# Optimization experiments

Hardware: AMD Instinct MI355X
Metric: run time of the kernel (lower is better)

## Reference

```python
import jax, jax.numpy as jnp
import numpy as np

NUM_ITERATIONS = 3
LN_EPS = 1e-5


def setup_inputs() -> dict:
    key = jax.random.key(0)
    ks = jax.random.split(key, 10)
    B, L, Lv, H = 8, 2048, 256, 1024
    s = 1.0 / np.sqrt(H)
    s2 = 1.0 / np.sqrt(2 * H)
    return {
        "text_feat": jax.random.normal(ks[0], (B, L, H), dtype=jnp.float32),
        "vision_feat": jax.random.normal(ks[1], (B, Lv, H), dtype=jnp.float32),
        "Wt": jax.random.uniform(ks[2], (H, H), jnp.float32, -s, s),
        "bt": jax.random.uniform(ks[3], (H,), jnp.float32, -s, s),
        "Wv": jax.random.uniform(ks[4], (H, H), jnp.float32, -s, s),
        "bv": jax.random.uniform(ks[5], (H,), jnp.float32, -s, s),
        "Wg": jax.random.uniform(ks[6], (H, 2 * H), jnp.float32, -s2, s2),
        "bg": jax.random.uniform(ks[7], (H,), jnp.float32, -s2, s2),
        "gamma": jnp.ones((H,), jnp.float32),
        "beta": jnp.zeros((H,), jnp.float32),
    }


def reference(text_feat, vision_feat, Wt, bt, Wv, bv, Wg, bg, gamma, beta):
    B, L, H = text_feat.shape
    # mean-pool vision over its sequence, broadcast over L
    vision_pooled = jnp.mean(vision_feat, axis=1, keepdims=True)          # [B,1,H]
    text_proj = jnp.einsum('blh,oh->blo', text_feat, Wt) + bt             # [B,L,H]
    vision_proj = jnp.einsum('bkh,oh->bko', vision_pooled, Wv) + bv       # [B,1,H]
    vision_proj = jnp.broadcast_to(vision_proj, (B, L, H))                # expand to [B,L,H]

    # agreement is loop-invariant in the original code; compute once
    agreement = jnp.sum(text_proj * vision_proj, axis=-1, keepdims=True)  # [B,L,1]

    coupling = jnp.zeros((B, L, 1), dtype=text_feat.dtype)
    fused = text_feat
    for _ in range(NUM_ITERATIONS):
        routing_weights = jax.nn.softmax(coupling, axis=1)                # softmax over L
        weighted_vision = routing_weights * vision_proj                   # [B,L,H]
        # gate = sigmoid(Linear(concat(text_proj, weighted_vision)))
        Wg_t, Wg_v = Wg[:, :H], Wg[:, H:]
        gate_pre = (jnp.einsum('blh,oh->blo', text_proj, Wg_t)
                    + jnp.einsum('blh,oh->blo', weighted_vision, Wg_v) + bg)
        gate = jax.nn.sigmoid(gate_pre)
        fused = text_feat + gate * weighted_vision
        coupling = coupling + agreement

    # LayerNorm over last dim (dropout is identity in eval)
    mu = jnp.mean(fused, axis=-1, keepdims=True)
    var = jnp.mean(jnp.square(fused - mu), axis=-1, keepdims=True)
    out = (fused - mu) / jnp.sqrt(var + LN_EPS) * gamma + beta
    return out
```

## Files before the change

kernel.cpp:

```cpp
#include <hip/hip_runtime.h>
#include <hip/hip_bf16.h>
#include <hip/hip_fp8.h>

typedef __bf16 bf16_t;
typedef bf16_t bf16x4 __attribute__((ext_vector_type(4)));
typedef bf16_t bf16x8 __attribute__((ext_vector_type(8)));
typedef float  f32x4  __attribute__((ext_vector_type(4)));

#define B_  8
#define L_  2048
#define H_  1024
#define LV_ 256

typedef const __attribute__((address_space(1))) void* gptr_as1;
typedef __attribute__((address_space(3))) void* lptr_as3;

__device__ __forceinline__ void gload_lds16(void* lds_base, const void* gsrc) {
  __builtin_amdgcn_global_load_lds((gptr_as1)gsrc, (lptr_as3)lds_base, 16, 0, 0);
}
__device__ __forceinline__ void gload_lds4(void* lds_base, const void* gsrc) {
  __builtin_amdgcn_global_load_lds((gptr_as1)gsrc, (lptr_as3)lds_base, 4, 0, 0);
}

__device__ __forceinline__ unsigned char to_fp8(float x) {
  return __hip_fp8_e4m3(x).__x;
}

__global__ __launch_bounds__(256) void vpool64(const float* __restrict__ vf,
                                               float* __restrict__ pooled) {
  __shared__ float part[256];
  int bid = blockIdx.x;
  int b = bid >> 3, hc = bid & 7;
  int t = threadIdx.x;
  int h = hc * 128 + (t & 127);
  int kh = t >> 7;
  const float* p = vf + (long)b * (LV_ * H_) + (long)kh * 128 * H_ + h;
  float s = 0.f;
  #pragma unroll 4
  for (int k = 0; k < 128; ++k) s += p[k * H_];
  part[t] = s;
  __syncthreads();
  if (t < 128)
    pooled[b * H_ + hc * 128 + t] = (part[t] + part[t + 128]) * (1.f / 256.f);
}

__global__ void matvec8(const float* __restrict__ W, int ldw, int woff,
                        const float* __restrict__ x,
                        const float* __restrict__ bias,
                        float* __restrict__ out) {
  int wid = threadIdx.x >> 6, lane = threadIdx.x & 63;
  int o = blockIdx.x * 4 + wid;
  const float* wr = W + (long)o * ldw + woff;
  float acc[B_];
  #pragma unroll
  for (int b = 0; b < B_; ++b) acc[b] = 0.f;
  for (int j = 0; j < 16; ++j) {
    float w = wr[lane + 64 * j];
    #pragma unroll
    for (int b = 0; b < B_; ++b) acc[b] += w * x[b * H_ + lane + 64 * j];
  }
  #pragma unroll
  for (int b = 0; b < B_; ++b)
    for (int off = 32; off; off >>= 1) acc[b] += __shfl_down(acc[b], off);
  if (lane == 0) {
    float bb = bias ? bias[o] : 0.f;
    #pragma unroll
    for (int b = 0; b < B_; ++b) out[b * H_ + o] = acc[b] + bb;
  }
}

__global__ __launch_bounds__(256) void smallops(const float* __restrict__ Wg,
                                                const float* __restrict__ Wt,
                                                const float* __restrict__ vp,
                                                const float* __restrict__ bt,
                                                const float* __restrict__ bg,
                                                float* __restrict__ gv,
                                                float* __restrict__ partU,
                                                float* __restrict__ cbb) {
  int bid = blockIdx.x;
  if (bid < 256) {
    int wid = threadIdx.x >> 6, lane = threadIdx.x & 63;
    int o = bid * 4 + wid;
    const float* wr = Wg + (long)o * 2048 + 1024;
    float acc[B_];
    #pragma unroll
    for (int b = 0; b < B_; ++b) acc[b] = 0.f;
    for (int j = 0; j < 16; ++j) {
      float w = wr[lane + 64 * j];
      #pragma unroll
      for (int b = 0; b < B_; ++b) acc[b] += w * vp[b * H_ + lane + 64 * j];
    }
    #pragma unroll
    for (int b = 0; b < B_; ++b)
      for (int off = 32; off; off >>= 1) acc[b] += __shfl_down(acc[b], off);
    if (lane == 0) {
      #pragma unroll
      for (int b = 0; b < B_; ++b) gv[b * H_ + o] = acc[b];
    }
  } else if (bid < 512) {
    int lb = bid - 256;
    int e = (lb & 3) * 256 + threadIdx.x;
    int oc = lb >> 2;
    float a[B_];
    #pragma unroll
    for (int b = 0; b < B_; ++b) a[b] = 0.f;
    #pragma unroll
    for (int i = 0; i < 16; ++i) {
      int o = oc * 16 + i;
      float w = Wt[(long)o * H_ + e];
      #pragma unroll
      for (int b = 0; b < B_; ++b) a[b] += w * vp[b * H_ + o];
    }
    #pragma unroll
    for (int b = 0; b < B_; ++b) partU[oc * 8192 + b * 1024 + e] = a[b];
  } else {
    int lb = bid - 512;
    int wid = threadIdx.x >> 6, lane = threadIdx.x & 63;
    int o = lb * 4 + wid;
    const float* wr = Wg + (long)o * 2048;
    float acc = 0.f;
    for (int j = 0; j < 16; ++j) acc += wr[lane + 64 * j] * bt[lane + 64 * j];
    for (int off = 32; off; off >>= 1) acc += __shfl_down(acc, off);
    if (lane == 0) cbb[o] = acc + bg[o];
  }
}

__global__ __launch_bounds__(256) void reduceK(const float* __restrict__ src,
                                               float* __restrict__ dst,
                                               int nc, float scale) {
  int j = blockIdx.x * 256 + threadIdx.x;
  float s = 0.f;
  for (int c = 0; c < nc; ++c) s += src[c * 8192 + j];
  dst[j] = s * scale;
}

__global__ __launch_bounds__(256) void cvt_pack(const float* __restrict__ text,
                                                const float* __restrict__ u,
                                                const float* __restrict__ Wt,
                                                unsigned char* __restrict__ t8p,
                                                float* __restrict__ agr,
                                                bf16_t* __restrict__ WtT) {
  int bid = blockIdx.x;
  int t = threadIdx.x;
  if (bid < 1024) {
    __shared__ unsigned char q8[16][1032];
    __shared__ float dred[4][16];
    int b = bid >> 7;
    int wid = t >> 6, lane = t & 63;
    const float4* trow = (const float4*)(text + (long)bid * (16 * H_));
    float4 uu = ((const float4*)(u + b * H_))[t];
    #pragma unroll 4
    for (int i = 0; i < 16; ++i) {
      float4 v = trow[i * 256 + t];
      float d = v.x * uu.x + v.y * uu.y + v.z * uu.z + v.w * uu.w;
      for (int off = 32; off; off >>= 1) d += __shfl_down(d, off);
      if (!lane) dred[wid][i] = d;
      uchar4 q = { to_fp8(v.x), to_fp8(v.y), to_fp8(v.z), to_fp8(v.w) };
      *(uchar4*)&q8[i][t * 4] = q;
    }
    __syncthreads();
    if (t < 16)
      agr[bid * 16 + t] = dred[0][t] + dred[1][t] + dred[2][t] + dred[3][t];
    unsigned char* dst = t8p + (long)bid * 16384;
    #pragma unroll
    for (int c = 0; c < 8; ++c) {
      int kb = wid * 8 + c;
      uint2 r = *(const uint2*)&q8[lane & 15][kb * 32 + (lane >> 4) * 8];
      *(uint2*)(dst + kb * 512 + lane * 8) = r;
    }
  } else {
    __shared__ float tile[64][65];
    int lb = bid - 1024;
    int hr = (lb >> 4) * 64;
    int ec = (lb & 15) * 64;
    int lr = t >> 4, lc = t & 15;
    #pragma unroll
    for (int rr = 0; rr < 4; ++rr) {
      int r = rr * 16 + lr;
      float4 v = *(const float4*)(Wt + (long)(hr + r) * H_ + ec + lc * 4);
      tile[r][lc * 4 + 0] = v.x; tile[r][lc * 4 + 1] = v.y;
      tile[r][lc * 4 + 2] = v.z; tile[r][lc * 4 + 3] = v.w;
    }
    __syncthreads();
    #pragma unroll
    for (int rr = 0; rr < 4; ++rr) {
      int er = rr * 16 + lr;
      bf16x4 o = { (bf16_t)tile[lc * 4 + 0][er], (bf16_t)tile[lc * 4 + 1][er],
                   (bf16_t)tile[lc * 4 + 2][er], (bf16_t)tile[lc * 4 + 3][er] };
      *(bf16x4*)(WtT + (long)(ec + er) * H_ + hr + lc * 4) = o;
    }
  }
}

__global__ __launch_bounds__(256) void wc_sm(const float* __restrict__ Wg,
                                             const bf16_t* __restrict__ Bt,
                                             unsigned char* __restrict__ Cw8,
                                             const float* __restrict__ ag,
                                             float* __restrict__ r) {
  __shared__ __align__(16) char lds[2][16384];
  __shared__ float red[4];
  if (blockIdx.x >= 256) {
    int b = blockIdx.x - 256, t = threadIdx.x;
    int wid = t >> 6, lane = t & 63;
    const float* a = ag + (long)b * L_;
    float v[8];
    float mx = -1e30f;
    #pragma unroll
    for (int j = 0; j < 8; ++j) { v[j] = 2.f * a[t + 256 * j]; mx = fmaxf(mx, v[j]); }
    for (int off = 32; off; off >>= 1) mx = fmaxf(mx, __shfl_down(mx, off));
    if (!lane) red[wid] = mx;
    __syncthreads();
    mx = fmaxf(fmaxf(red[0], red[1]), fmaxf(red[2], red[3]));
    __syncthreads();
    float sum = 0.f;
    #pragma unroll
    for (int j = 0; j < 8; ++j) { v[j] = __expf(v[j] - mx); sum += v[j]; }
    for (int off = 32; off; off >>= 1) sum += __shfl_down(sum, off);
    if (!lane) red[wid] = sum;
    __syncthreads();
    sum = red[0] + red[1] + red[2] + red[3];
    float inv = 1.f / sum;
    #pragma unroll
    for (int j = 0; j < 8; ++j) r[(long)b * L_ + t + 256 * j] = v[j] * inv;
    return;
  }
  const int tid = threadIdx.x;
  const int wid = tid >> 6, lane = tid & 63;
  const int fr = lane & 15, fkb = (lane >> 4) * 16, fq = (lane >> 4) * 4;
  const int wm = wid >> 1, wn = wid & 1;
  const int tm = blockIdx.x & 15, tn = blockIdx.x >> 4;
  const int m0 = tm * 64, n0 = tn * 64;

  const int d0 = tid * 16;
  const int p  = d0 ^ (((d0 >> 7) & 7) << 4);
  const int rS = p >> 7, cS = (p & 127) >> 1;

  const int swz = (fr & 7) << 4;
  const int e0 = fkb ^ swz;
  const int e1 = (64 + fkb) ^ swz;

  auto stage = [&](int t) {
    char* base = lds[t & 1];
    gload_lds16(base + 8192 + d0,        Bt + (long)(n0 + rS) * H_ + t * 64 + cS);
    gload_lds16(base + 8192 + 4096 + d0, Bt + (long)(n0 + 32 + rS) * H_ + t * 64 + cS);
    const float* a0 = Wg + (long)(m0 + rS) * 2048 + t * 64 + cS;
    const float* a1 = Wg + (long)(m0 + 32 + rS) * 2048 + t * 64 + cS;
    float4 x0 = *(const float4*)a0, x1 = *(const float4*)(a0 + 4);
    float4 y0 = *(const float4*)a1, y1 = *(const float4*)(a1 + 4);
    bf16x8 bx = { (bf16_t)x0.x, (bf16_t)x0.y, (bf16_t)x0.z, (bf16_t)x0.w,
                  (bf16_t)x1.x, (bf16_t)x1.y, (bf16_t)x1.z, (bf16_t)x1.w };
    bf16x8 by = { (bf16_t)y0.x, (bf16_t)y0.y, (bf16_t)y0.z, (bf16_t)y0.w,
                  (bf16_t)y1.x, (bf16_t)y1.y, (bf16_t)y1.z, (bf16_t)y1.w };
    *(bf16x8*)(base + d0) = bx;
    *(bf16x8*)(base + 4096 + d0) = by;
  };

  f32x4 acc[2][2];
  #pragma unroll
  for (int m = 0; m < 2; ++m)
    #pragma unroll
    for (int n = 0; n < 2; ++n) acc[m][n] = (f32x4){0.f, 0.f, 0.f, 0.f};

  stage(0);
  __syncthreads();
  for (int t = 0; t < 16; ++t) {
    if (t + 1 < 16) stage(t + 1);
    char* buf = lds[t & 1];
    char* AR = buf + (wm * 32 + fr) * 128;
    char* BR = buf + 8192 + (wn * 32 + fr) * 128;
    bf16x8 a[2][2], b[2][2];
    #pragma unroll
    for (int m = 0; m < 2; ++m) {
      a[m][0] = *(const bf16x8*)(AR + m * 2048 + e0);
      a[m][1] = *(const bf16x8*)(AR + m * 2048 + e1);
      b[m][0] = *(const bf16x8*)(BR + m * 2048 + e0);
      b[m][1] = *(const bf16x8*)(BR + m * 2048 + e1);
    }
    #pragma unroll
    for (int m = 0; m < 2; ++m)
      #pragma unroll
      for (int n = 0; n < 2; ++n) {
        acc[m][n] = __builtin_amdgcn_mfma_f32_16x16x32_bf16(a[m][0], b[n][0], acc[m][n], 0, 0, 0);
        acc[m][n] = __builtin_amdgcn_mfma_f32_16x16x32_bf16(a[m][1], b[n][1], acc[m][n], 0, 0, 0);
      }
    __syncthreads();
  }
  #pragma unroll
  for (int m = 0; m < 2; ++m)
    #pragma unroll
    for (int r_ = 0; r_ < 4; ++r_) {
      int row = m0 + wm * 32 + m * 16 + fq + r_;
      #pragma unroll
      for (int n = 0; n < 2; ++n) {
        int col = n0 + wn * 32 + n * 16 + fr;
        Cw8[((row >> 4) * 32 + (col >> 5)) * 512
            + ((row & 15) + (((col >> 3) & 3) << 4)) * 8 + (col & 7)]
          = to_fp8(acc[m][n][r_] * 16.f);
      }
    }
}

#define BOFF 16777216
__global__ __launch_bounds__(512, 2)
void gemm_ln(const unsigned char* __restrict__ AB,
             const float* __restrict__ textf,
             const float* __restrict__ cbb, const float* __restrict__ rbuf,
             const float* __restrict__ gvb, const float* __restrict__ vpb,
             const float* __restrict__ gamma, const float* __restrict__ beta,
             float* __restrict__ out) {
  extern __shared__ __align__(16) char dlds[];
  const int tid  = threadIdx.x;
  const int w    = tid >> 6;
  const int lane = tid & 63;
  const int fr   = lane & 15;
  const int fq   = (lane >> 4) * 4;
  const int bid  = blockIdx.x;
  const long m0  = (long)bid * 64;
  const int bat  = (int)(m0 >> 11);

  const int o0 = tid * 4;
  const unsigned char* aSrc = AB + (long)bid * 65536 + (o0 >> 9) * 16384 + (o0 & 511);
  const unsigned char* bSrc = AB + BOFF + (long)(tid >> 5) * 16384 + (tid & 31) * 16;
  const int bD = (tid >> 5) * 512 + (tid & 31) * 16;

  {
    char* P = dlds + 104448;
    if (tid < 256) {
      gload_lds16(P + tid * 16,          cbb + tid * 4);
      gload_lds16(P + 8192 + tid * 16,   vpb + bat * H_ + tid * 4);
      gload_lds16(P + 16384 + tid * 16,  beta + tid * 4);
    } else {
      int t2 = tid - 256;
      gload_lds16(P + 4096 + t2 * 16,    gvb + bat * H_ + t2 * 4);
      gload_lds16(P + 12288 + t2 * 16,   gamma + t2 * 4);
    }
  }

  f32x4 acc[4][8];
  #pragma unroll
  for (int m = 0; m < 4; ++m)
    #pragma unroll
    for (int n = 0; n < 8; ++n) acc[m][n] = (f32x4){0.f, 0.f, 0.f, 0.f};

#define STAGE(t)                                                        \
  {                                                                     \
    gload_lds4(dlds + ((t) % 3) * 2048 + o0, aSrc + (t) * 512);         \
    _Pragma("unroll")                                                   \
    for (int r_ = 0; r_ < 4; ++r_)                                      \
      gload_lds16(dlds + 6144 + ((t) % 3) * 32768 + r_ * 8192 + bD,     \
                  bSrc + (long)r_ * 262144 + (t) * 512);                \
  }
#define KITER(t, WN)                                                    \
  {                                                                     \
    __builtin_amdgcn_sched_barrier(0);                                  \
    asm volatile("s_waitcnt vmcnt(" #WN ")" ::: "memory");              \
    __builtin_amdgcn_s_barrier();                                       \
    __builtin_amdgcn_sched_barrier(0);                                  \
    if ((t) + 2 < 32) STAGE((t) + 2)                                    \
    const char* Ab_ = dlds + ((t) % 3) * 2048 + lane * 8;               \
    const char* Bb_ = dlds + 6144 + ((t) % 3) * 32768 + w * 4096        \
                           + lane * 8;                                  \
    long a_[4], b_[8];                                                  \
    _Pragma("unroll")                                                   \
    for (int m_ = 0; m_ < 4; ++m_)                                      \
      a_[m_] = *(const long*)(Ab_ + m_ * 512);                          \
    _Pragma("unroll")                                                   \
    for (int n_ = 0; n_ < 8; ++n_)                                      \
      b_[n_] = *(const long*)(Bb_ + n_ * 512);                          \
    _Pragma("unroll")                                                   \
    for (int m_ = 0; m_ < 4; ++m_)                                      \
      _Pragma("unroll")                                                 \
      for (int n_ = 0; n_ < 8; ++n_)                                    \
        acc[m_][n_] = __builtin_amdgcn_mfma_f32_16x16x32_fp8_fp8(       \
            a_[m_], b_[n_], acc[m_][n_], 0, 0, 0);                      \
  }

  STAGE(0)
  asm volatile("" ::: "memory");
  STAGE(1)

  KITER(0, 5)  KITER(1, 5)  KITER(2, 5)  KITER(3, 5)
  KITER(4, 5)  KITER(5, 5)  KITER(6, 5)  KITER(7, 5)
  KITER(8, 5)  KITER(9, 5)  KITER(10, 5) KITER(11, 5)
  KITER(12, 5) KITER(13, 5) KITER(14, 5) KITER(15, 5)
  KITER(16, 5) KITER(17, 5) KITER(18, 5) KITER(19, 5)
  KITER(20, 5) KITER(21, 5) KITER(22, 5) KITER(23, 5)
  KITER(24, 5) KITER(25, 5) KITER(26, 5) KITER(27, 5)
  KITER(28, 5) KITER(29, 5) KITER(30, 5) KITER(31, 0)
#undef KITER
#undef STAGE

  const int lr = tid >> 5;
  const int jj = tid & 31;
  char* P = dlds + 104448;

  #pragma unroll
  for (int m = 0; m < 4; ++m) {
    __syncthreads();
    #pragma unroll
    for (int n = 0; n < 8; ++n) {
      #pragma unroll
      for (int r = 0; r < 4; ++r) {
        int rl = fq + r;
        int c  = (w * 128 + n * 16 + fr) ^ (((rl >> 2) & 3) << 4);
        *(float*)(dlds + rl * 4096 + c * 4) = acc[m][n][r];
      }
    }
    __syncthreads();
    long row = m0 + m * 16 + lr;
    float rv = rbuf[row];
    const float* tf = textf + row * H_;
    const int rot = ((lr >> 2) & 3) << 4;
    float s = 0.f, q = 0.f;
    #pragma unroll 2
    for (int k = 0; k < 8; ++k) {
      int c0 = k * 128 + jj * 4;
      char* slot = dlds + lr * 4096 + ((c0 ^ rot) * 4);
      f32x4 a4 = *(const f32x4*)slot;
      float4 t4  = *(const float4*)(tf + c0);
      f32x4 cb4 = *(const f32x4*)(P + c0 * 4);
      f32x4 gv4 = *(const f32x4*)(P + 4096 + c0 * 4);
      f32x4 vp4 = *(const f32x4*)(P + 8192 + c0 * 4);
      f32x4 f4;
      float gp, g;
      gp = a4[0] * 0.0625f + cb4[0] + rv * gv4[0];
      g = 1.f / (1.f + __expf(-gp));
      f4[0] = t4.x + g * rv * vp4[0];
      gp = a4[1] * 0.0625f + cb4[1] + rv * gv4[1];
      g = 1.f / (1.f + __expf(-gp));
      f4[1] = t4.y + g * rv * vp4[1];
      gp = a4[2] * 0.0625f + cb4[2] + rv * gv4[2];
      g = 1.f / (1.f + __expf(-gp));
      f4[2] = t4.z + g * rv * vp4[2];
      gp = a4[3] * 0.0625f + cb4[3] + rv * gv4[3];
      g = 1.f / (1.f + __expf(-gp));
      f4[3] = t4.w + g * rv * vp4[3];
      *(f32x4*)slot = f4;
      s += f4[0] + f4[1] + f4[2] + f4[3];
      q += f4[0] * f4[0] + f4[1] * f4[1] + f4[2] * f4[2] + f4[3] * f4[3];
    }
    #pragma unroll
    for (int off = 1; off < 32; off <<= 1) {
      s += __shfl_xor(s, off);
      q += __shfl_xor(q, off);
    }
    float mu  = s * (1.f / H_);
    float var = q * (1.f / H_) - mu * mu;
    float inv = rsqrtf(var + 1e-5f);
    float* op = out + row * H_;
    #pragma unroll 2
    for (int k = 0; k < 8; ++k) {
      int c0 = k * 128 + jj * 4;
      f32x4 f4 = *(const f32x4*)(dlds + lr * 4096 + ((c0 ^ rot) * 4));
      f32x4 gg = *(const f32x4*)(P + 12288 + c0 * 4);
      f32x4 bb = *(const f32x4*)(P + 16384 + c0 * 4);
      float4 o4;
      o4.x = (f4[0] - mu) * inv * gg[0] + bb[0];
      o4.y = (f4[1] - mu) * inv * gg[1] + bb[1];
      o4.z = (f4[2] - mu) * inv * gg[2] + bb[2];
      o4.w = (f4[3] - mu) * inv * gg[3] + bb[3];
      *(float4*)(op + c0) = o4;
    }
  }
}

extern "C" void kernel_launch(void* const* d_in, const int* in_sizes, int n_in,
                              void* d_out, int out_size, void* d_ws, size_t ws_size,
                              hipStream_t stream) {
  const float* text  = (const float*)d_in[0];
  const float* vis   = (const float*)d_in[1];
  const float* Wt    = (const float*)d_in[2];
  const float* bt    = (const float*)d_in[3];
  const float* Wv    = (const float*)d_in[4];
  const float* bv    = (const float*)d_in[5];
  const float* Wg    = (const float*)d_in[6];
  const float* bg    = (const float*)d_in[7];
  const float* gamma = (const float*)d_in[8];
  const float* beta  = (const float*)d_in[9];
  float* out = (float*)d_out;

  char* ws = (char*)d_ws;
  unsigned char* t8p   = (unsigned char*)(ws);
  unsigned char* Wc8p  = (unsigned char*)(ws + (size_t)16777216);
  bf16_t* WtT_b = (bf16_t*)(ws + (size_t)17825792);
  float*  pooled = (float*)(ws + (size_t)19922944);
  float*  vp     = (float*)(ws + (size_t)19955712);
  float*  gv     = (float*)(ws + (size_t)19988480);
  float*  u      = (float*)(ws + (size_t)20021248);
  float*  cbb    = (float*)(ws + (size_t)20054016);
  float*  rbuf   = (float*)(ws + (size_t)20058112);
  float*  agr    = (float*)(ws + (size_t)20123648);
  float*  partU  = (float*)(ws + (size_t)20189184);

  static bool smem_set = false;
  if (!smem_set) {
    (void)hipFuncSetAttribute((const void*)gemm_ln,
                              hipFuncAttributeMaxDynamicSharedMemorySize, 125184);
    smem_set = true;
  }

  vpool64<<<64, 256, 0, stream>>>(vis, pooled);
  matvec8<<<256, 256, 0, stream>>>(Wv, 1024, 0, pooled, bv, vp);
  smallops<<<768, 256, 0, stream>>>(Wg, Wt, vp, bt, bg, gv, partU, cbb);
  reduceK<<<32, 256, 0, stream>>>(partU, u, 64, 1.f);

  cvt_pack<<<1280, 256, 0, stream>>>(text, u, Wt, t8p, agr, WtT_b);
  wc_sm<<<264, 256, 0, stream>>>(Wg, WtT_b, Wc8p, agr, rbuf);

  gemm_ln<<<256, 512, 125184, stream>>>(t8p, text, cbb, rbuf, gv, vp,
                                        gamma, beta, out);
}
```

Measured before the change: 120.4 us.

## Merge prep kernels, use atomics for u, fold softmax into GEMM epilogue

Cuts the launch chain from seven kernels to five. The Wt transpose and the cbb bias dot move into the same launch as vision pooling, and that launch also zeroes u. The partial sums for u are now accumulated with atomicAdd, which removes the reduceK kernel and the partU buffer. The fp8 packing of text and the Wc GEMM share one launch, and each gemm_ln block recomputes its batch's softmax over agreement from agr instead of reading a precomputed routing buffer. The aim is to remove launch and serialization overhead. The costs are redundant softmax work in every GEMM block, atomic contention on u, and an order-dependent float sum.

```diff
diff --git a/kernel.cpp b/kernel.cpp
--- a/kernel.cpp
+++ b/kernel.cpp
@@ -26,22 +26,65 @@
   return __hip_fp8_e4m3(x).__x;
 }
 
-__global__ __launch_bounds__(256) void vpool64(const float* __restrict__ vf,
-                                               float* __restrict__ pooled) {
-  __shared__ float part[256];
+__global__ __launch_bounds__(256) void prep1(const float* __restrict__ vf,
+                                             const float* __restrict__ Wt,
+                                             const float* __restrict__ Wg,
+                                             const float* __restrict__ bt,
+                                             const float* __restrict__ bg,
+                                             float* __restrict__ pooled,
+                                             bf16_t* __restrict__ WtT,
+                                             float* __restrict__ cbb,
+                                             float* __restrict__ u) {
+  __shared__ __align__(16) char shm[16640];
   int bid = blockIdx.x;
-  int b = bid >> 3, hc = bid & 7;
   int t = threadIdx.x;
-  int h = hc * 128 + (t & 127);
-  int kh = t >> 7;
-  const float* p = vf + (long)b * (LV_ * H_) + (long)kh * 128 * H_ + h;
-  float s = 0.f;
-  #pragma unroll 4
-  for (int k = 0; k < 128; ++k) s += p[k * H_];
-  part[t] = s;
-  __syncthreads();
-  if (t < 128)
-    pooled[b * H_ + hc * 128 + t] = (part[t] + part[t + 128]) * (1.f / 256.f);
+  if (bid < 64) {
+    float* part = (float*)shm;
+    int b = bid >> 3, hc = bid & 7;
+    int h = hc * 128 + (t & 127);
+    int kh = t >> 7;
+    const float* p = vf + (long)b * (LV_ * H_) + (long)kh * 128 * H_ + h;
+    float s = 0.f;
+    #pragma unroll 4
+    for (int k = 0; k < 128; ++k) s += p[k * H_];
+    part[t] = s;
+    __syncthreads();
+    if (t < 128)
+      pooled[b * H_ + hc * 128 + t] = (part[t] + part[t + 128]) * (1.f / 256.f);
+  } else if (bid < 320) {
+    float (*tile)[65] = (float(*)[65])shm;
+    int lb = bid - 64;
+    int hr = (lb >> 4) * 64;
+    int ec = (lb & 15) * 64;
+    int lr = t >> 4, lc = t & 15;
+    #pragma unroll
+    for (int rr = 0; rr < 4; ++rr) {
+      int r = rr * 16 + lr;
+      float4 v = *(const float4*)(Wt + (long)(hr + r) * H_ + ec + lc * 4);
+      tile[r][lc * 4 + 0] = v.x; tile[r][lc * 4 + 1] = v.y;
+      tile[r][lc * 4 + 2] = v.z; tile[r][lc * 4 + 3] = v.w;
+    }
+    __syncthreads();
+    #pragma unroll
+    for (int rr = 0; rr < 4; ++rr) {
+      int er = rr * 16 + lr;
+      bf16x4 o = { (bf16_t)tile[lc * 4 + 0][er], (bf16_t)tile[lc * 4 + 1][er],
+                   (bf16_t)tile[lc * 4 + 2][er], (bf16_t)tile[lc * 4 + 3][er] };
+      *(bf16x4*)(WtT + (long)(ec + er) * H_ + hr + lc * 4) = o;
+    }
+  } else if (bid < 576) {
+    int lb = bid - 320;
+    int wid = t >> 6, lane = t & 63;
+    int o = lb * 4 + wid;
+    const float* wr = Wg + (long)o * 2048;
+    float acc = 0.f;
+    for (int j = 0; j < 16; ++j) acc += wr[lane + 64 * j] * bt[lane + 64 * j];
+    for (int off = 32; off; off >>= 1) acc += __shfl_down(acc, off);
+    if (lane == 0) cbb[o] = acc + bg[o];
+  } else {
+    int z = bid - 576;
+    *(float4*)(u + z * 1024 + t * 4) = (float4){0.f, 0.f, 0.f, 0.f};
+  }
 }
 
 __global__ void matvec8(const float* __restrict__ W, int ldw, int woff,
@@ -69,17 +112,15 @@
   }
 }
 
-__global__ __launch_bounds__(256) void smallops(const float* __restrict__ Wg,
-                                                const float* __restrict__ Wt,
-                                                const float* __restrict__ vp,
-                                                const float* __restrict__ bt,
-                                                const float* __restrict__ bg,
-                                                float* __restrict__ gv,
-                                                float* __restrict__ partU,
-                                                float* __restrict__ cbb) {
+__global__ __launch_bounds__(256) void prep3(const float* __restrict__ Wg,
+                                             const float* __restrict__ Wt,
+                                             const float* __restrict__ vp,
+                                             float* __restrict__ gv,
+                                             float* __restrict__ u) {
   int bid = blockIdx.x;
+  int t = threadIdx.x;
   if (bid < 256) {
-    int wid = threadIdx.x >> 6, lane = threadIdx.x & 63;
+    int wid = t >> 6, lane = t & 63;
     int o = bid * 4 + wid;
     const float* wr = Wg + (long)o * 2048 + 1024;
     float acc[B_];
@@ -97,9 +138,9 @@
       #pragma unroll
       for (int b = 0; b < B_; ++b) gv[b * H_ + o] = acc[b];
     }
-  } else if (bid < 512) {
+  } else {
     int lb = bid - 256;
-    int e = (lb & 3) * 256 + threadIdx.x;
+    int e = (lb & 3) * 256 + t;
     int oc = lb >> 2;
     float a[B_];
     #pragma unroll
@@ -112,39 +153,23 @@
       for (int b = 0; b < B_; ++b) a[b] += w * vp[b * H_ + o];
     }
     #pragma unroll
-    for (int b = 0; b < B_; ++b) partU[oc * 8192 + b * 1024 + e] = a[b];
-  } else {
-    int lb = bid - 512;
-    int wid = threadIdx.x >> 6, lane = threadIdx.x & 63;
-    int o = lb * 4 + wid;
-    const float* wr = Wg + (long)o * 2048;
-    float acc = 0.f;
-    for (int j = 0; j < 16; ++j) acc += wr[lane + 64 * j] * bt[lane + 64 * j];
-    for (int off = 32; off; off >>= 1) acc += __shfl_down(acc, off);
-    if (lane == 0) cbb[o] = acc + bg[o];
-  }
-}
-
-__global__ __launch_bounds__(256) void reduceK(const float* __restrict__ src,
-                                               float* __restrict__ dst,
-                                               int nc, float scale) {
-  int j = blockIdx.x * 256 + threadIdx.x;
-  float s = 0.f;
-  for (int c = 0; c < nc; ++c) s += src[c * 8192 + j];
-  dst[j] = s * scale;
-}
-
-__global__ __launch_bounds__(256) void cvt_pack(const float* __restrict__ text,
-                                                const float* __restrict__ u,
-                                                const float* __restrict__ Wt,
-                                                unsigned char* __restrict__ t8p,
-                                                float* __restrict__ agr,
-                                                bf16_t* __restrict__ WtT) {
+    for (int b = 0; b < B_; ++b) atomicAdd(u + b * 1024 + e, a[b]);
+  }
+}
+
+__global__ __launch_bounds__(256) void cvt_wc(const float* __restrict__ text,
+                                              const float* __restrict__ u,
+                                              const float* __restrict__ Wg,
+                                              const bf16_t* __restrict__ Bt,
+                                              unsigned char* __restrict__ t8p,
+                                              float* __restrict__ agr,
+                                              unsigned char* __restrict__ Cw8) {
+  __shared__ __align__(16) char shm[32800];
   int bid = blockIdx.x;
   int t = threadIdx.x;
   if (bid < 1024) {
-    __shared__ unsigned char q8[16][1032];
-    __shared__ float dred[4][16];
+    unsigned char (*q8)[1032] = (unsigned char(*)[1032])shm;
+    float (*dred)[16] = (float(*)[16])(shm + 16512);
     int b = bid >> 7;
     int wid = t >> 6, lane = t & 63;
     const float4* trow = (const float4*)(text + (long)bid * (16 * H_));
@@ -168,68 +193,19 @@
       uint2 r = *(const uint2*)&q8[lane & 15][kb * 32 + (lane >> 4) * 8];
       *(uint2*)(dst + kb * 512 + lane * 8) = r;
     }
-  } else {
-    __shared__ float tile[64][65];
-    int lb = bid - 1024;
-    int hr = (lb >> 4) * 64;
-    int ec = (lb & 15) * 64;
-    int lr = t >> 4, lc = t & 15;
-    #pragma unroll
-    for (int rr = 0; rr < 4; ++rr) {
-      int r = rr * 16 + lr;
-      float4 v = *(const float4*)(Wt + (long)(hr + r) * H_ + ec + lc * 4);
-      tile[r][lc * 4 + 0] = v.x; tile[r][lc * 4 + 1] = v.y;
-      tile[r][lc * 4 + 2] = v.z; tile[r][lc * 4 + 3] = v.w;
-    }
-    __syncthreads();
-    #pragma unroll
-    for (int rr = 0; rr < 4; ++rr) {
-      int er = rr * 16 + lr;
-      bf16x4 o = { (bf16_t)tile[lc * 4 + 0][er], (bf16_t)tile[lc * 4 + 1][er],
-                   (bf16_t)tile[lc * 4 + 2][er], (bf16_t)tile[lc * 4 + 3][er] };
-      *(bf16x4*)(WtT + (long)(ec + er) * H_ + hr + lc * 4) = o;
-    }
-  }
-}
-
-__global__ __launch_bounds__(256) void wc_sm(const float* __restrict__ Wg,
-                                             const bf16_t* __restrict__ Bt,
-                                             unsigned char* __restrict__ Cw8,
-                                             const float* __restrict__ ag,
-                                             float* __restrict__ r) {
-  __shared__ __align__(16) char lds[2][16384];
-  __shared__ float red[4];
-  if (blockIdx.x >= 256) {
-    int b = blockIdx.x - 256, t = threadIdx.x;
-    int wid = t >> 6, lane = t & 63;
-    const float* a = ag + (long)b * L_;
-    float v[8];
-    float mx = -1e30f;
-    #pragma unroll
-    for (int j = 0; j < 8; ++j) { v[j] = 2.f * a[t + 256 * j]; mx = fmaxf(mx, v[j]); }
-    for (int off = 32; off; off >>= 1) mx = fmaxf(mx, __shfl_down(mx, off));
-    if (!lane) red[wid] = mx;
-    __syncthreads();
-    mx = fmaxf(fmaxf(red[0], red[1]), fmaxf(red[2], red[3]));
-    __syncthreads();
-    float sum = 0.f;
-    #pragma unroll
-    for (int j = 0; j < 8; ++j) { v[j] = __expf(v[j] - mx); sum += v[j]; }
-    for (int off = 32; off; off >>= 1) sum += __shfl_down(sum, off);
-    if (!lane) red[wid] = sum;
-    __syncthreads();
-    sum = red[0] + red[1] + red[2] + red[3];
-    float inv = 1.f / sum;
-    #pragma unroll
-    for (int j = 0; j < 8; ++j) r[(long)b * L_ + t + 256 * j] = v[j] * inv;
     return;
   }
-  const int tid = threadIdx.x;
+  const int tid = t;
   const int wid = tid >> 6, lane = tid & 63;
   const int fr = lane & 15, fkb = (lane >> 4) * 16, fq = (lane >> 4) * 4;
   const int wm = wid >> 1, wn = wid & 1;
-  const int tm = blockIdx.x & 15, tn = blockIdx.x >> 4;
+  const int lb = bid - 1024;
+  const int tm = lb & 15, tn = lb >> 4;
   const int m0 = tm * 64, n0 = tn * 64;
+
+  char* ldsA = shm;
+  float* red = (float*)(shm + 32768);
+  (void)red;
 
   const int d0 = tid * 16;
   const int p  = d0 ^ (((d0 >> 7) & 7) << 4);
@@ -239,12 +215,12 @@
   const int e0 = fkb ^ swz;
   const int e1 = (64 + fkb) ^ swz;
 
-  auto stage = [&](int t) {
-    char* base = lds[t & 1];
-    gload_lds16(base + 8192 + d0,        Bt + (long)(n0 + rS) * H_ + t * 64 + cS);
-    gload_lds16(base + 8192 + 4096 + d0, Bt + (long)(n0 + 32 + rS) * H_ + t * 64 + cS);
-    const float* a0 = Wg + (long)(m0 + rS) * 2048 + t * 64 + cS;
-    const float* a1 = Wg + (long)(m0 + 32 + rS) * 2048 + t * 64 + cS;
+  auto stage = [&](int tt) {
+    char* base = ldsA + (tt & 1) * 16384;
+    gload_lds16(base + 8192 + d0,        Bt + (long)(n0 + rS) * H_ + tt * 64 + cS);
+    gload_lds16(base + 8192 + 4096 + d0, Bt + (long)(n0 + 32 + rS) * H_ + tt * 64 + cS);
+    const float* a0 = Wg + (long)(m0 + rS) * 2048 + tt * 64 + cS;
+    const float* a1 = Wg + (long)(m0 + 32 + rS) * 2048 + tt * 64 + cS;
     float4 x0 = *(const float4*)a0, x1 = *(const float4*)(a0 + 4);
     float4 y0 = *(const float4*)a1, y1 = *(const float4*)(a1 + 4);
     bf16x8 bx = { (bf16_t)x0.x, (bf16_t)x0.y, (bf16_t)x0.z, (bf16_t)x0.w,
@@ -263,9 +239,9 @@
 
   stage(0);
   __syncthreads();
-  for (int t = 0; t < 16; ++t) {
-    if (t + 1 < 16) stage(t + 1);
-    char* buf = lds[t & 1];
+  for (int tt = 0; tt < 16; ++tt) {
+    if (tt + 1 < 16) stage(tt + 1);
+    char* buf = ldsA + (tt & 1) * 16384;
     char* AR = buf + (wm * 32 + fr) * 128;
     char* BR = buf + 8192 + (wn * 32 + fr) * 128;
     bf16x8 a[2][2], b[2][2];
@@ -304,7 +280,7 @@
 __global__ __launch_bounds__(512, 2)
 void gemm_ln(const unsigned char* __restrict__ AB,
              const float* __restrict__ textf,
-             const float* __restrict__ cbb, const float* __restrict__ rbuf,
+             const float* __restrict__ cbb, const float* __restrict__ agrb,
              const float* __restrict__ gvb, const float* __restrict__ vpb,
              const float* __restrict__ gamma, const float* __restrict__ beta,
              float* __restrict__ out) {
@@ -317,6 +293,31 @@
   const int bid  = blockIdx.x;
   const long m0  = (long)bid * 64;
   const int bat  = (int)(m0 >> 11);
+
+  {
+    float* red = (float*)(dlds + 124928);
+    float* rvA = (float*)(dlds + 124992);
+    float4 av = *(const float4*)(agrb + (long)bat * 2048 + tid * 4);
+    float mloc = fmaxf(fmaxf(av.x, av.y), fmaxf(av.z, av.w)) * 2.f;
+    #pragma unroll
+    for (int off = 32; off; off >>= 1) mloc = fmaxf(mloc, __shfl_xor(mloc, off));
+    if ((tid & 63) == 0) red[tid >> 6] = mloc;
+    __syncthreads();
+    float mx = red[0];
+    #pragma unroll
+    for (int i = 1; i < 8; ++i) mx = fmaxf(mx, red[i]);
+    float sl = __expf(2.f * av.x - mx) + __expf(2.f * av.y - mx)
+             + __expf(2.f * av.z - mx) + __expf(2.f * av.w - mx);
+    #pragma unroll
+    for (int off = 32; off; off >>= 1) sl += __shfl_xor(sl, off);
+    __syncthreads();
+    if ((tid & 63) == 0) red[tid >> 6] = sl;
+    __syncthreads();
+    float ssum = red[0] + red[1] + red[2] + red[3]
+               + red[4] + red[5] + red[6] + red[7];
+    if (tid < 64) rvA[tid] = __expf(2.f * agrb[m0 + tid] - mx) / ssum;
+    __syncthreads();
+  }
 
   const int o0 = tid * 4;
   const unsigned char* aSrc = AB + (long)bid * 65536 + (o0 >> 9) * 16384 + (o0 & 511);
@@ -393,6 +394,7 @@
   const int lr = tid >> 5;
   const int jj = tid & 31;
   char* P = dlds + 104448;
+  const float* rvA = (const float*)(dlds + 124992);
 
   #pragma unroll
   for (int m = 0; m < 4; ++m) {
@@ -408,7 +410,7 @@
     }
     __syncthreads();
     long row = m0 + m * 16 + lr;
-    float rv = rbuf[row];
+    float rv = rvA[m * 16 + lr];
     const float* tf = textf + row * H_;
     const int rot = ((lr >> 2) & 3) << 4;
     float s = 0.f, q = 0.f;
@@ -488,25 +490,19 @@
   float*  gv     = (float*)(ws + (size_t)19988480);
   float*  u      = (float*)(ws + (size_t)20021248);
   float*  cbb    = (float*)(ws + (size_t)20054016);
-  float*  rbuf   = (float*)(ws + (size_t)20058112);
   float*  agr    = (float*)(ws + (size_t)20123648);
-  float*  partU  = (float*)(ws + (size_t)20189184);
 
   static bool smem_set = false;
   if (!smem_set) {
     (void)hipFuncSetAttribute((const void*)gemm_ln,
-                              hipFuncAttributeMaxDynamicSharedMemorySize, 125184);
+                              hipFuncAttributeMaxDynamicSharedMemorySize, 125440);
     smem_set = true;
   }
 
-  vpool64<<<64, 256, 0, stream>>>(vis, pooled);
+  prep1<<<584, 256, 0, stream>>>(vis, Wt, Wg, bt, bg, pooled, WtT_b, cbb, u);
   matvec8<<<256, 256, 0, stream>>>(Wv, 1024, 0, pooled, bv, vp);
-  smallops<<<768, 256, 0, stream>>>(Wg, Wt, vp, bt, bg, gv, partU, cbb);
-  reduceK<<<32, 256, 0, stream>>>(partU, u, 64, 1.f);
-
-  cvt_pack<<<1280, 256, 0, stream>>>(text, u, Wt, t8p, agr, WtT_b);
-  wc_sm<<<264, 256, 0, stream>>>(Wg, WtT_b, Wc8p, agr, rbuf);
-
-  gemm_ln<<<256, 512, 125184, stream>>>(t8p, text, cbb, rbuf, gv, vp,
+  prep3<<<512, 256, 0, stream>>>(Wg, Wt, vp, gv, u);
+  cvt_wc<<<1280, 256, 0, stream>>>(text, u, Wg, WtT_b, t8p, agr, Wc8p);
+  gemm_ln<<<256, 512, 125440, stream>>>(t8p, text, cbb, agr, gv, vp,
                                         gamma, beta, out);
 }
```

Measured after the change: 99.93 us. 17.0% less time.
